# Kernel optimization log

Hardware: AMD Instinct MI355X
Metric: run time of the kernel (lower is better)

## Reference

```python
import jax, jax.numpy as jnp
import numpy as np

T, D, E, K = 8192, 4096, 64, 8


def setup_inputs() -> dict:
    key = jax.random.key(0)
    k1, k2, k3, k4 = jax.random.split(key, 4)
    x = jax.random.normal(k1, (T, D), dtype=jnp.float32)
    # nn.Linear stores weight as [out_features, in_features]
    Wg = jax.random.normal(k2, (E, D), dtype=jnp.float32) * (1.0 / np.sqrt(D))
    Wc = jax.random.normal(k3, (E, D), dtype=jnp.float32) * (1.0 / np.sqrt(D))
    extra_scale = jnp.zeros((E,), dtype=jnp.float32)  # init zeros as in module
    extra_bias = jax.random.normal(k4, (E,), dtype=jnp.float32) * 0.01
    return {"x": x, "Wg": Wg, "Wc": Wc, "extra_scale": extra_scale,
            "extra_bias": extra_bias, "topk": K}


def reference(x, Wg, Wc, extra_scale, extra_bias, topk):
    # scores = |classifier(x) * silu(gate(x))|, softmax in fp32
    gate = jnp.einsum('td,ed->te', x, Wg)        # [T, E]
    cls = jnp.einsum('td,ed->te', x, Wc)         # [T, E]
    scores = jnp.abs(cls * jax.nn.silu(gate))
    scores = jax.nn.softmax(scores.astype(jnp.float32), axis=-1)
    biased = scores + extra_bias[None, :]        # load-balance bias, used only for selection
    _, indices = jax.lax.top_k(biased, topk)     # [T, K]
    original = 1.0 + scores * extra_scale[None, :]
    weights = jnp.take_along_axis(original, indices, axis=1)  # [T, K]
    return weights.astype(x.dtype), indices
```

## Files before the change

### kernel.cpp

```cpp
#include <hip/hip_runtime.h>
#include <math.h>


#define T_DIM 8192
#define D_DIM 4096
#define E_DIM 64
#define N2    128
#define KTOP  8
#define MB_ROWS 64

typedef __attribute__((ext_vector_type(8)))  short bfrag8;
typedef __attribute__((ext_vector_type(16))) float f32x16;

__device__ __forceinline__ unsigned short f2bf_rne(float f) {
    unsigned int u = __float_as_uint(f);
    unsigned int r = u + 0x7fffu + ((u >> 16) & 1u);
    return (unsigned short)(r >> 16);
}
__device__ __forceinline__ float bf2f(unsigned short h) {
    return __uint_as_float(((unsigned int)h) << 16);
}
__device__ __forceinline__ void split3(float v, unsigned short& h,
                                       unsigned short& m, unsigned short& l) {
    h = f2bf_rne(v);
    const float r1 = v - bf2f(h);
    m = f2bf_rne(r1);
    const float r2 = r1 - bf2f(m);
    l = f2bf_rne(r2);
}

__device__ __forceinline__ void gload16(const void* g, void* l) {
    __builtin_amdgcn_global_load_lds(
        (const __attribute__((address_space(1))) void*)g,
        (__attribute__((address_space(3))) void*)l, 16, 0, 0);
}

__global__ __launch_bounds__(256)
void router_prep(const float* __restrict__ Wg, const float* __restrict__ Wc,
                 unsigned short* __restrict__ Wpk)
{
    const int t   = blockIdx.x * 256 + threadIdx.x;
    const int col = t >> 9;
    const int ch  = t & 511;
    const int k   = ch << 3;

    const float* src = (col < E_DIM) ? (Wg + (size_t)col * D_DIM)
                                     : (Wc + (size_t)(col - E_DIM) * D_DIM);
    const float4 w0 = ((const float4*)(src + k))[0];
    const float4 w1 = ((const float4*)(src + k))[1];
    const float v[8] = {w0.x, w0.y, w0.z, w0.w, w1.x, w1.y, w1.z, w1.w};

    unsigned short hv[8], mv[8], lv[8];
    #pragma unroll
    for (int j = 0; j < 8; ++j) split3(v[j], hv[j], mv[j], lv[j]);

    const int k32 = k >> 5, h2 = (k >> 4) & 1, lh = (k >> 3) & 1;
    const int n = col >> 5, lane = lh * 32 + (col & 31);
    const size_t base = ((((size_t)k32 * 4 + n) * 3 + 0) * 2 + h2) * 512 + (size_t)lane * 8;
    *(ushort4*)(Wpk + base)          = make_ushort4(hv[0], hv[1], hv[2], hv[3]);
    *(ushort4*)(Wpk + base + 4)      = make_ushort4(hv[4], hv[5], hv[6], hv[7]);
    *(ushort4*)(Wpk + base + 1024)   = make_ushort4(mv[0], mv[1], mv[2], mv[3]);
    *(ushort4*)(Wpk + base + 1028)   = make_ushort4(mv[4], mv[5], mv[6], mv[7]);
    *(ushort4*)(Wpk + base + 2048)   = make_ushort4(lv[0], lv[1], lv[2], lv[3]);
    *(ushort4*)(Wpk + base + 2052)   = make_ushort4(lv[4], lv[5], lv[6], lv[7]);
}

__global__ __launch_bounds__(512, 4)
void router_gemm(const float* __restrict__ x,
                 const unsigned short* __restrict__ Wpk,
                 float* __restrict__ P,
                 int sliceK)
{
    __shared__ float sA[2][MB_ROWS * 32];

    const int tid  = threadIdx.x;
    const int lane = tid & 63;
    const int wid  = tid >> 6;
    const int wr   = wid >> 2;
    const int wc   = wid & 3;
    const int l31  = lane & 31;
    const int lh   = lane >> 5;
    const int mb   = blockIdx.x;
    const int ks   = blockIdx.y;
    const int k0   = ks * sliceK;
    const int NT   = sliceK >> 5;
    const int brow0 = mb * MB_ROWS;
    const int rl   = wr * 32 + l31;
    const int sw   = l31 & 7;

    f32x16 acc;
    #pragma unroll
    for (int r = 0; r < 16; ++r) acc[r] = 0.f;

    #define STAGE(bf_, kk_)                                                      \
        {                                                                        \
            const int chunk_ = tid;                                              \
            const int row_   = chunk_ >> 3;                                      \
            const int csrc_  = (chunk_ & 7) ^ (row_ & 7);                        \
            const float* gp_ = x + (size_t)(brow0 + row_) * D_DIM                \
                                 + (kk_) + csrc_ * 4;                            \
            gload16(gp_, &sA[bf_][chunk_ * 4]);                                  \
        }

    STAGE(0, k0);
    __syncthreads();

    for (int t = 0; t < NT; ++t) {
        const int kk = k0 + t * 32;
        const int bf = t & 1;

        if (t + 1 < NT) STAGE(bf ^ 1, kk + 32);

        bfrag8 ah[2], am[2], al[2];
        #pragma unroll
        for (int h2 = 0; h2 < 2; ++h2) {
            const int c0 = h2 * 4 + lh * 2;
            const float4 q0 = *(const float4*)&sA[bf][rl * 32 + ((c0    ) ^ sw) * 4];
            const float4 q1 = *(const float4*)&sA[bf][rl * 32 + ((c0 + 1) ^ sw) * 4];
            const float f[8] = {q0.x, q0.y, q0.z, q0.w, q1.x, q1.y, q1.z, q1.w};
            #pragma unroll
            for (int j = 0; j < 8; ++j) {
                unsigned short h, m, l;
                split3(f[j], h, m, l);
                ah[h2][j] = (short)h; am[h2][j] = (short)m; al[h2][j] = (short)l;
            }
        }

        const size_t k32 = (size_t)(kk >> 5);
        #pragma unroll
        for (int h2 = 0; h2 < 2; ++h2) {
            const unsigned short* bb =
                Wpk + ((((k32 * 4 + wc) * 3 + 0) * 2 + h2) * 64 + lane) * 8;
            const bfrag8 bh = *(const bfrag8*)(bb);
            const bfrag8 bm = *(const bfrag8*)(bb + 1024);
            const bfrag8 bl = *(const bfrag8*)(bb + 2048);
            acc = __builtin_amdgcn_mfma_f32_32x32x16_bf16(ah[h2], bl, acc, 0, 0, 0);
            acc = __builtin_amdgcn_mfma_f32_32x32x16_bf16(al[h2], bh, acc, 0, 0, 0);
            acc = __builtin_amdgcn_mfma_f32_32x32x16_bf16(am[h2], bm, acc, 0, 0, 0);
            acc = __builtin_amdgcn_mfma_f32_32x32x16_bf16(ah[h2], bm, acc, 0, 0, 0);
            acc = __builtin_amdgcn_mfma_f32_32x32x16_bf16(am[h2], bh, acc, 0, 0, 0);
            acc = __builtin_amdgcn_mfma_f32_32x32x16_bf16(ah[h2], bh, acc, 0, 0, 0);
        }

        __syncthreads();
    }

    float* Pb = P + ((size_t)ks * T_DIM + brow0 + wr * 32) * N2 + wc * 32 + l31;
    #pragma unroll
    for (int r = 0; r < 16; ++r) {
        const int wrow = (r & 3) + 8 * (r >> 2) + 4 * lh;
        Pb[(size_t)wrow * N2] = acc[r];
    }
    #undef STAGE
}

__global__ __launch_bounds__(256)
void router_topk(const float* __restrict__ P,
                 const float* __restrict__ scale,
                 const float* __restrict__ bias,
                 float* __restrict__ out,
                 int ksplit)
{
    const int lane = threadIdx.x & 63;
    const int wid  = threadIdx.x >> 6;
    const int row  = blockIdx.x * 4 + wid;

    float g = 0.f, c = 0.f;
    for (int ks = 0; ks < ksplit; ++ks) {
        const float* p = P + ((size_t)ks * T_DIM + row) * N2;
        g += p[lane];
        c += p[E_DIM + lane];
    }
    const float sg = g / (1.f + expf(-g));
    const float v  = fabsf(c * sg);

    float m = v;
    #pragma unroll
    for (int off = 32; off >= 1; off >>= 1) m = fmaxf(m, __shfl_xor(m, off));
    const float e = expf(v - m);
    float Z = e;
    #pragma unroll
    for (int off = 32; off >= 1; off >>= 1) Z += __shfl_xor(Z, off);
    const float s = e / Z;

    const float sc  = scale[lane];
    float cur = s + bias[lane];

    float myw = 0.f; int myi = 0;
    #pragma unroll
    for (int j = 0; j < KTOP; ++j) {
        float bv = cur; int bi = lane;
        #pragma unroll
        for (int off = 32; off >= 1; off >>= 1) {
            const float ov = __shfl_xor(bv, off);
            const int   oi = __shfl_xor(bi, off);
            if (ov > bv || (ov == bv && oi < bi)) { bv = ov; bi = oi; }
        }
        const float s_bi  = __shfl(s,  bi);
        const float sc_bi = __shfl(sc, bi);
        const float w = 1.f + s_bi * sc_bi;
        if (lane == j)  { myw = w; myi = bi; }
        if (lane == bi) cur = -INFINITY;
    }

    if (lane < KTOP) {
        out[(size_t)row * KTOP + lane] = myw;
        out[(size_t)T_DIM * KTOP + (size_t)row * KTOP + lane] = (float)myi;
    }
}

extern "C" void kernel_launch(void* const* d_in, const int* in_sizes, int n_in,
                              void* d_out, int out_size, void* d_ws, size_t ws_size,
                              hipStream_t stream)
{
    const float* x  = (const float*)d_in[0];
    const float* Wg = (const float*)d_in[1];
    const float* Wc = (const float*)d_in[2];
    const float* sc = (const float*)d_in[3];
    const float* bs = (const float*)d_in[4];
    float* out = (float*)d_out;
    float* P   = (float*)d_ws;

    const size_t PER = (size_t)T_DIM * N2 * sizeof(float);
    const size_t WSP = (size_t)N2 * D_DIM * sizeof(unsigned short);

    int S = 8;
    while (S > 1 && (size_t)S * PER + 3 * WSP > ws_size) S >>= 1;
    const int sliceK = D_DIM / S;

    unsigned short* Wpk = (unsigned short*)((char*)d_ws + (size_t)S * PER);

    router_prep<<<256, 256, 0, stream>>>(Wg, Wc, Wpk);
    router_gemm<<<dim3(T_DIM / MB_ROWS, S), 512, 0, stream>>>(x, Wpk, P, sliceK);
    router_topk<<<T_DIM / 4, 256, 0, stream>>>(P, sc, bs, out, S);
}
```

Measured before the change: 278.3 us.

## Split x into bf16 triples once per tile in LDS instead of per wave

The GEMM block drops from 64 rows and 8 waves to 32 rows and 4 waves. Each thread now loads x through registers, splits it into hi/mid/lo bf16 once, and writes the pieces into LDS already in MFMA fragment layout, so waves read the fragments directly. Before, each of the four column waves re-split the same A rows, so the split arithmetic ran four times per element. The cost is that the async global-to-LDS load is replaced by a register prefetch, and the smaller tiles mean the packed weights are reloaded for twice as many row blocks.

```diff
diff --git a/kernel.cpp b/kernel.cpp
--- a/kernel.cpp
+++ b/kernel.cpp
@@ -7,7 +7,7 @@
 #define E_DIM 64
 #define N2    128
 #define KTOP  8
-#define MB_ROWS 64
+#define MB_ROWS 32
 
 typedef __attribute__((ext_vector_type(8)))  short bfrag8;
 typedef __attribute__((ext_vector_type(16))) float f32x16;
@@ -27,12 +27,6 @@
     m = f2bf_rne(r1);
     const float r2 = r1 - bf2f(m);
     l = f2bf_rne(r2);
-}
-
-__device__ __forceinline__ void gload16(const void* g, void* l) {
-    __builtin_amdgcn_global_load_lds(
-        (const __attribute__((address_space(1))) void*)g,
-        (__attribute__((address_space(3))) void*)l, 16, 0, 0);
 }
 
 __global__ __launch_bounds__(256)
@@ -65,19 +59,17 @@
     *(ushort4*)(Wpk + base + 2052)   = make_ushort4(lv[4], lv[5], lv[6], lv[7]);
 }
 
-__global__ __launch_bounds__(512, 4)
+__global__ __launch_bounds__(256, 4)
 void router_gemm(const float* __restrict__ x,
                  const unsigned short* __restrict__ Wpk,
                  float* __restrict__ P,
                  int sliceK)
 {
-    __shared__ float sA[2][MB_ROWS * 32];
+    __shared__ unsigned short sF[2][3][2][64][8];
 
     const int tid  = threadIdx.x;
     const int lane = tid & 63;
-    const int wid  = tid >> 6;
-    const int wr   = wid >> 2;
-    const int wc   = wid & 3;
+    const int wc   = tid >> 6;
     const int l31  = lane & 31;
     const int lh   = lane >> 5;
     const int mb   = blockIdx.x;
@@ -85,48 +77,53 @@
     const int k0   = ks * sliceK;
     const int NT   = sliceK >> 5;
     const int brow0 = mb * MB_ROWS;
-    const int rl   = wr * 32 + l31;
-    const int sw   = l31 & 7;
+
+    const int srow = tid >> 3;
+    const int kq   = tid & 7;
+    const int h2w  = kq >> 2;
+    const int lew  = ((kq >> 1) & 1) * 32 + srow;
+    const int jw   = (kq & 1) * 4;
+    const float* gsrc = x + (size_t)(brow0 + srow) * D_DIM + kq * 4;
 
     f32x16 acc;
     #pragma unroll
     for (int r = 0; r < 16; ++r) acc[r] = 0.f;
 
-    #define STAGE(bf_, kk_)                                                      \
+    #define WRITE_TILE(v_, bf_)                                                  \
         {                                                                        \
-            const int chunk_ = tid;                                              \
-            const int row_   = chunk_ >> 3;                                      \
-            const int csrc_  = (chunk_ & 7) ^ (row_ & 7);                        \
-            const float* gp_ = x + (size_t)(brow0 + row_) * D_DIM                \
-                                 + (kk_) + csrc_ * 4;                            \
-            gload16(gp_, &sA[bf_][chunk_ * 4]);                                  \
-        }
-
-    STAGE(0, k0);
+            ushort4 hv_, mv_, lv_;                                               \
+            unsigned short h_, m_, l_;                                           \
+            split3((v_).x, h_, m_, l_); hv_.x = h_; mv_.x = m_; lv_.x = l_;      \
+            split3((v_).y, h_, m_, l_); hv_.y = h_; mv_.y = m_; lv_.y = l_;      \
+            split3((v_).z, h_, m_, l_); hv_.z = h_; mv_.z = m_; lv_.z = l_;      \
+            split3((v_).w, h_, m_, l_); hv_.w = h_; mv_.w = m_; lv_.w = l_;      \
+            *(ushort4*)&sF[bf_][0][h2w][lew][jw] = hv_;                          \
+            *(ushort4*)&sF[bf_][1][h2w][lew][jw] = mv_;                          \
+            *(ushort4*)&sF[bf_][2][h2w][lew][jw] = lv_;                          \
+        }
+
+    {
+        const float4 v0 = *(const float4*)(gsrc + k0);
+        WRITE_TILE(v0, 0);
+    }
     __syncthreads();
 
     for (int t = 0; t < NT; ++t) {
-        const int kk = k0 + t * 32;
         const int bf = t & 1;
-
-        if (t + 1 < NT) STAGE(bf ^ 1, kk + 32);
+        const bool more = (t + 1 < NT);
+
+        float4 nx;
+        if (more) nx = *(const float4*)(gsrc + k0 + (t + 1) * 32);
 
         bfrag8 ah[2], am[2], al[2];
         #pragma unroll
         for (int h2 = 0; h2 < 2; ++h2) {
-            const int c0 = h2 * 4 + lh * 2;
-            const float4 q0 = *(const float4*)&sA[bf][rl * 32 + ((c0    ) ^ sw) * 4];
-            const float4 q1 = *(const float4*)&sA[bf][rl * 32 + ((c0 + 1) ^ sw) * 4];
-            const float f[8] = {q0.x, q0.y, q0.z, q0.w, q1.x, q1.y, q1.z, q1.w};
-            #pragma unroll
-            for (int j = 0; j < 8; ++j) {
-                unsigned short h, m, l;
-                split3(f[j], h, m, l);
-                ah[h2][j] = (short)h; am[h2][j] = (short)m; al[h2][j] = (short)l;
-            }
-        }
-
-        const size_t k32 = (size_t)(kk >> 5);
+            ah[h2] = *(const bfrag8*)&sF[bf][0][h2][lane][0];
+            am[h2] = *(const bfrag8*)&sF[bf][1][h2][lane][0];
+            al[h2] = *(const bfrag8*)&sF[bf][2][h2][lane][0];
+        }
+
+        const size_t k32 = (size_t)((k0 + t * 32) >> 5);
         #pragma unroll
         for (int h2 = 0; h2 < 2; ++h2) {
             const unsigned short* bb =
@@ -142,16 +139,17 @@
             acc = __builtin_amdgcn_mfma_f32_32x32x16_bf16(ah[h2], bh, acc, 0, 0, 0);
         }
 
+        if (more) WRITE_TILE(nx, bf ^ 1);
         __syncthreads();
     }
-
-    float* Pb = P + ((size_t)ks * T_DIM + brow0 + wr * 32) * N2 + wc * 32 + l31;
+    #undef WRITE_TILE
+
+    float* Pb = P + ((size_t)ks * T_DIM + brow0) * N2 + wc * 32 + l31;
     #pragma unroll
     for (int r = 0; r < 16; ++r) {
         const int wrow = (r & 3) + 8 * (r >> 2) + 4 * lh;
         Pb[(size_t)wrow * N2] = acc[r];
     }
-    #undef STAGE
 }
 
 __global__ __launch_bounds__(256)
@@ -231,6 +229,6 @@
     unsigned short* Wpk = (unsigned short*)((char*)d_ws + (size_t)S * PER);
 
     router_prep<<<256, 256, 0, stream>>>(Wg, Wc, Wpk);
-    router_gemm<<<dim3(T_DIM / MB_ROWS, S), 512, 0, stream>>>(x, Wpk, P, sliceK);
+    router_gemm<<<dim3(T_DIM / MB_ROWS, S), 256, 0, stream>>>(x, Wpk, P, sliceK);
     router_topk<<<T_DIM / 4, 256, 0, stream>>>(P, sc, bs, out, S);
 }
```

Result: faster. 265.7 us (-4.5%).
